# Kernel optimization log

Measured on AMD Instinct MI355X. Metric: run time of the kernel, lower is better.

Reference implementation:

```python
import jax, jax.numpy as jnp
import numpy as np

N = 8000        # nodes
E = 64000       # directed edges (before self-loops)
F_IN = 3201     # node_dim=1 + encoding_dim(128)*25
N_TRAIN = 4000


def setup_inputs() -> dict:
    key = jax.random.key(0)
    k = jax.random.split(key, 4)
    d = {
        'x': jax.random.normal(k[0], (N, F_IN), dtype=jnp.float32),
        'edge_index': jax.random.randint(k[1], (2, E), 0, N),
        'y': jax.random.uniform(k[2], (N,), dtype=jnp.float32),
        'train_idx': jax.random.randint(k[3], (N_TRAIN,), 0, N),
    }
    cnt = [0]
    def w(shape, fan_in):
        cnt[0] += 1
        kk = jax.random.fold_in(jax.random.key(1), cnt[0])
        return (jax.random.normal(kk, shape, dtype=jnp.float32) / np.float32(np.sqrt(fan_in)))
    ones = lambda n: jnp.ones((n,), jnp.float32)
    zeros = lambda n: jnp.zeros((n,), jnp.float32)
    d['bn0_g'] = ones(F_IN); d['bn0_b'] = zeros(F_IN)
    d['W1l'] = w((F_IN, 1024), F_IN); d['W1r'] = w((F_IN, 1024), F_IN)
    d['a1'] = w((2, 512), 512); d['b1'] = zeros(1024)
    d['bn1_g'] = ones(1024); d['bn1_b'] = zeros(1024)
    d['W2l'] = w((1024, 512), 1024); d['W2r'] = w((1024, 512), 1024)
    d['a2'] = w((1, 512), 512); d['b2'] = zeros(512)
    d['bn2_g'] = ones(512); d['bn2_b'] = zeros(512)
    d['W3l'] = w((512, 512), 512); d['W3r'] = w((512, 512), 512)
    d['a3'] = w((1, 512), 512); d['b3'] = zeros(512)
    d['bn3_g'] = ones(512); d['bn3_b'] = zeros(512)
    d['W4l'] = w((512, 512), 512); d['W4r'] = w((512, 512), 512)
    d['a4'] = w((1, 512), 512); d['b4'] = zeros(512)
    d['Wh'] = w((512, 1), 512); d['bh'] = zeros(1)
    return d


def _batchnorm(h, g, b, eps=1e-5):
    # training-mode batch statistics over the node dim
    m = h.mean(axis=0)
    v = h.var(axis=0)
    return (h - m) * jax.lax.rsqrt(v + jnp.float32(eps)) * g + b


def _gatv2(h, src, dst, Wl, Wr, att, bias, n):
    # GATv2Conv with concat heads, softmax over incoming edges, aggr='mean'
    H, C = att.shape
    xl = (h @ Wl).reshape(n, H, C)   # source transform
    xr = (h @ Wr).reshape(n, H, C)   # target transform
    z = jax.nn.leaky_relu(xl[src] + xr[dst], negative_slope=0.2)  # [E,H,C]
    e = jnp.einsum('ehc,hc->eh', z, att)                          # [E,H]
    emax = jax.ops.segment_max(e, dst, num_segments=n)            # segment softmax
    ex = jnp.exp(e - emax[dst])
    denom = jax.ops.segment_sum(ex, dst, num_segments=n)
    alpha = ex / denom[dst]
    agg = jax.ops.segment_sum(alpha[:, :, None] * xl[src], dst, num_segments=n)
    deg = jax.ops.segment_sum(jnp.ones(src.shape[0], h.dtype), dst, num_segments=n)
    return (agg / deg[:, None, None]).reshape(n, H * C) + bias


def reference(x, edge_index, y, train_idx, bn0_g, bn0_b, W1l, W1r, a1, b1,
              bn1_g, bn1_b, W2l, W2r, a2, b2, bn2_g, bn2_b, W3l, W3r, a3, b3,
              bn3_g, bn3_b, W4l, W4r, a4, b4, Wh, bh):
    n = x.shape[0]
    loops = jnp.arange(n, dtype=edge_index.dtype)  # PyG add_self_loops=True
    src = jnp.concatenate([edge_index[0], loops])
    dst = jnp.concatenate([edge_index[1], loops])
    h = _batchnorm(x, bn0_g, bn0_b)
    h = _gatv2(h, src, dst, W1l, W1r, a1, b1, n)          # -> [N,1024]
    h = jax.nn.relu(_batchnorm(h, bn1_g, bn1_b))
    h = _gatv2(h, src, dst, W2l, W2r, a2, b2, n)          # -> [N,512]
    h = jax.nn.relu(_batchnorm(h, bn2_g, bn2_b))
    h = _gatv2(h, src, dst, W3l, W3r, a3, b3, n)
    h = jax.nn.relu(_batchnorm(h, bn3_g, bn3_b))
    h = jax.nn.relu(_gatv2(h, src, dst, W4l, W4r, a4, b4, n))
    pred = jax.nn.sigmoid(h @ Wh + bh)[:, 0]              # [N]
    return pred[train_idx], y[train_idx]
```

## Files before the change

kernel.cpp:

```cpp
#include <hip/hip_runtime.h>
#include <math.h>

typedef __bf16 bf16x8 __attribute__((ext_vector_type(8)));
typedef float f32x4 __attribute__((ext_vector_type(4)));
typedef unsigned short ushort8 __attribute__((ext_vector_type(8)));

__device__ __forceinline__ float bf2f(unsigned short u) {
  union { unsigned int i; float f; } c; c.i = ((unsigned int)u) << 16; return c.f;
}
__device__ __forceinline__ unsigned short f2bf(float f) {
  union { float f; unsigned int i; } c; c.f = f;
  unsigned int r = (c.i + 0x7fffu + ((c.i >> 16) & 1u)) >> 16;
  return (unsigned short)r;
}

__global__ void deg_init_k(int* deg, int n) {
  int i = blockIdx.x * blockDim.x + threadIdx.x;
  if (i < n) deg[i] = 1;
}

__global__ void deg_count_k(const int* __restrict__ dst, int* __restrict__ deg, int e) {
  int i = blockIdx.x * blockDim.x + threadIdx.x;
  if (i < e) atomicAdd(&deg[dst[i]], 1);
}

__global__ void scan_k(const int* __restrict__ deg, int* __restrict__ offsets,
                       int* __restrict__ cursor, int n) {
  __shared__ int sums[1024];
  int tid = threadIdx.x;
  int chunk = (n + 1023) >> 10;
  int base = tid * chunk;
  int s = 0;
  for (int i = 0; i < chunk; ++i) {
    int j = base + i;
    if (j < n) s += deg[j];
  }
  sums[tid] = s;
  __syncthreads();
  for (int off = 1; off < 1024; off <<= 1) {
    int v = (tid >= off) ? sums[tid - off] : 0;
    __syncthreads();
    sums[tid] += v;
    __syncthreads();
  }
  int run = sums[tid] - s;
  for (int i = 0; i < chunk; ++i) {
    int j = base + i;
    if (j < n) {
      offsets[j] = run;
      cursor[j] = run;
      run += deg[j];
    }
  }
  if (tid == 1023) offsets[n] = sums[1023];
}

__global__ void csr_fill_k(const int* __restrict__ src, const int* __restrict__ dst,
                           int* __restrict__ cursor, int* __restrict__ csr_src,
                           int e, int n) {
  int i = blockIdx.x * blockDim.x + threadIdx.x;
  if (i >= e + n) return;
  int s, d;
  if (i < e) { s = src[i]; d = dst[i]; }
  else       { s = i - e;  d = s; }
  int pos = atomicAdd(&cursor[d], 1);
  csr_src[pos] = s;
}

__global__ __launch_bounds__(256)
void stats_convert_k(const float* __restrict__ x, unsigned short* __restrict__ Abf,
                     float* __restrict__ s1, float* __restrict__ s2,
                     int M, int K, int Kp) {
  int c = blockIdx.x * 256 + threadIdx.x;
  if (c >= Kp) return;
  int rows = (M + gridDim.y - 1) / gridDim.y;
  int r0 = blockIdx.y * rows;
  int r1 = min(M, r0 + rows);
  if (c >= K) {
    for (int r = r0; r < r1; ++r) Abf[(size_t)r * Kp + c] = 0;
    return;
  }
  float a = 0.f, b = 0.f;
  int r = r0;
  for (; r + 4 <= r1; r += 4) {
    float v0 = x[(size_t)(r + 0) * K + c];
    float v1 = x[(size_t)(r + 1) * K + c];
    float v2 = x[(size_t)(r + 2) * K + c];
    float v3 = x[(size_t)(r + 3) * K + c];
    a += v0 + v1 + v2 + v3;
    b += v0 * v0 + v1 * v1 + v2 * v2 + v3 * v3;
    Abf[(size_t)(r + 0) * Kp + c] = f2bf(v0);
    Abf[(size_t)(r + 1) * Kp + c] = f2bf(v1);
    Abf[(size_t)(r + 2) * Kp + c] = f2bf(v2);
    Abf[(size_t)(r + 3) * Kp + c] = f2bf(v3);
  }
  for (; r < r1; ++r) {
    float v = x[(size_t)r * K + c];
    a += v; b += v * v;
    Abf[(size_t)r * Kp + c] = f2bf(v);
  }
  atomicAdd(&s1[c], a);
  atomicAdd(&s2[c], b);
}

__global__ __launch_bounds__(256)
void col_stats_bf_k(const unsigned short* __restrict__ h, int M, int D,
                    float* __restrict__ s1, float* __restrict__ s2) {
  int c = blockIdx.x * 256 + threadIdx.x;
  if (c >= D) return;
  int rows = (M + gridDim.y - 1) / gridDim.y;
  int r0 = blockIdx.y * rows;
  int r1 = min(M, r0 + rows);
  float a = 0.f, b = 0.f;
  int r = r0;
  for (; r + 4 <= r1; r += 4) {
    float v0 = bf2f(h[(size_t)(r + 0) * D + c]);
    float v1 = bf2f(h[(size_t)(r + 1) * D + c]);
    float v2 = bf2f(h[(size_t)(r + 2) * D + c]);
    float v3 = bf2f(h[(size_t)(r + 3) * D + c]);
    a += v0 + v1 + v2 + v3;
    b += v0 * v0 + v1 * v1 + v2 * v2 + v3 * v3;
  }
  for (; r < r1; ++r) {
    float v = bf2f(h[(size_t)r * D + c]);
    a += v; b += v * v;
  }
  atomicAdd(&s1[c], a);
  atomicAdd(&s2[c], b);
}

__global__ void bn_fin_k(const float* __restrict__ s1, const float* __restrict__ s2,
                         const float* __restrict__ g, const float* __restrict__ b,
                         float* __restrict__ acol, float* __restrict__ ccol,
                         int D, float invM) {
  int c = blockIdx.x * blockDim.x + threadIdx.x;
  if (c >= D) return;
  float m = s1[c] * invM;
  float v = fmaxf(s2[c] * invM - m * m, 0.f);
  float a = rsqrtf(v + 1e-5f) * g[c];
  acol[c] = a;
  ccol[c] = b[c] - m * a;
}

__global__ __launch_bounds__(256)
void bn_apply8_k(const unsigned short* __restrict__ h, const float* __restrict__ acol,
                 const float* __restrict__ ccol, unsigned short* __restrict__ outb,
                 size_t total, int D) {
  size_t i = ((size_t)blockIdx.x * 256 + threadIdx.x) * 8;
  if (i >= total) return;
  ushort8 u = *(const ushort8*)(h + i);
  int c = (int)(i % (size_t)D);
  ushort8 o;
#pragma unroll
  for (int j = 0; j < 8; ++j) {
    float v = bf2f(u[j]) * acol[c + j] + ccol[c + j];
    o[j] = f2bf(fmaxf(v, 0.f));
  }
  *(ushort8*)(outb + i) = o;
}

__global__ __launch_bounds__(256)
void wconv_k(const float* __restrict__ W, unsigned short* __restrict__ WT,
             int K, int N, int Kp,
             const float* __restrict__ scale, const float* __restrict__ cshift,
             float* __restrict__ bias) {
  __shared__ float t[32][33];
  int n0 = blockIdx.x * 32, k0 = blockIdx.y * 32;
  int tx = threadIdx.x & 31, ty = threadIdx.x >> 5;
  float bsum = 0.f;
#pragma unroll
  for (int i = 0; i < 32; i += 8) {
    int k = k0 + ty + i, nn = n0 + tx;
    float v = (k < K && nn < N) ? W[(size_t)k * N + nn] : 0.f;
    t[ty + i][tx] = v;
    if (cshift && k < K) bsum += cshift[k] * v;
  }
  if (cshift) atomicAdd(&bias[n0 + tx], bsum);
  __syncthreads();
#pragma unroll
  for (int i = 0; i < 32; i += 8) {
    int nn = n0 + ty + i, k = k0 + tx;
    if (nn < N && k < Kp) {
      float v = t[tx][ty + i];
      if (scale && k < K) v *= scale[k];
      WT[(size_t)nn * Kp + k] = f2bf(v);
    }
  }
}

__global__ __launch_bounds__(256)
void gemm_bf16_k(const unsigned short* __restrict__ A,
                 const unsigned short* __restrict__ Bt,
                 unsigned short* __restrict__ outL, unsigned short* __restrict__ outR,
                 const float* __restrict__ bias, int M, int Nh, int K) {
  __shared__ unsigned short sA[128 * 64];
  __shared__ unsigned short sB[128 * 64];
  const int tid = threadIdx.x;
  const int wave = tid >> 6, lane = tid & 63;
  const int wm = wave >> 1, wn = wave & 1;
  const int l16 = lane & 15, lq = lane >> 4;
  const int row0 = blockIdx.y * 128, col0 = blockIdx.x * 128;

  f32x4 acc[4][4] = {};

  for (int kt = 0; kt < K; kt += 64) {
#pragma unroll
    for (int i = 0; i < 4; ++i) {
      int s = i * 256 + tid;
      int r = s >> 3;
      int g = (s & 7) ^ (r & 7);
      int ra = row0 + r;
      ra = ra < M ? ra : M - 1;
      const unsigned short* ga = A + (size_t)ra * K + (kt + g * 8);
      __builtin_amdgcn_global_load_lds(
          (const __attribute__((address_space(1))) void*)ga,
          (__attribute__((address_space(3))) void*)&sA[s * 8], 16, 0, 0);
      const unsigned short* gb = Bt + (size_t)(col0 + r) * K + (kt + g * 8);
      __builtin_amdgcn_global_load_lds(
          (const __attribute__((address_space(1))) void*)gb,
          (__attribute__((address_space(3))) void*)&sB[s * 8], 16, 0, 0);
    }
    __syncthreads();
#pragma unroll
    for (int ks = 0; ks < 2; ++ks) {
      bf16x8 af[4], bff[4];
#pragma unroll
      for (int t = 0; t < 4; ++t) {
        int g = ks * 4 + lq;
        int r = wm * 64 + t * 16 + l16;
        af[t] = *(const bf16x8*)&sA[(r * 8 + (g ^ (r & 7))) * 8];
        int rb = wn * 64 + t * 16 + l16;
        bff[t] = *(const bf16x8*)&sB[(rb * 8 + (g ^ (rb & 7))) * 8];
      }
#pragma unroll
      for (int mt = 0; mt < 4; ++mt)
#pragma unroll
        for (int nt = 0; nt < 4; ++nt)
          acc[mt][nt] = __builtin_amdgcn_mfma_f32_16x16x32_bf16(af[mt], bff[nt], acc[mt][nt], 0, 0, 0);
    }
    __syncthreads();
  }
#pragma unroll
  for (int mt = 0; mt < 4; ++mt) {
    int rbase = row0 + wm * 64 + mt * 16 + lq * 4;
#pragma unroll
    for (int nt = 0; nt < 4; ++nt) {
      int col = col0 + wn * 64 + nt * 16 + l16;
      float bv = bias ? bias[col] : 0.f;
      unsigned short* base;
      int cc;
      if (col < Nh) { base = outL; cc = col; }
      else          { base = outR; cc = col - Nh; }
#pragma unroll
      for (int r = 0; r < 4; ++r) {
        int rr = rbase + r;
        if (rr < M) base[(size_t)rr * Nh + cc] = f2bf(acc[mt][nt][r] + bv);
      }
    }
  }
}

template <int H>
__global__ __launch_bounds__(256)
void gat_edge_k(const unsigned short* __restrict__ xl, const unsigned short* __restrict__ xr,
                const float* __restrict__ att, const float* __restrict__ bias,
                const int* __restrict__ csr, const int* __restrict__ offsets,
                unsigned short* __restrict__ out, int n, int relu) {
  int gw = (blockIdx.x * 256 + threadIdx.x) >> 6;
  int lane = threadIdx.x & 63;
  if (gw >= n * H) return;
  int node = gw / H;
  int head = gw - node * H;
  const int W = H * 512;
  const size_t rowoff = (size_t)node * W + head * 512;
  int c0 = lane * 8;

  float xrv[8], atv[8];
  {
    ushort8 u = *(const ushort8*)(xr + rowoff + c0);
    const float* ap = att + head * 512 + c0;
#pragma unroll
    for (int j = 0; j < 8; ++j) { xrv[j] = bf2f(u[j]); atv[j] = ap[j]; }
  }
  float m = -1e30f, l = 0.f;
  float acc[8];
#pragma unroll
  for (int j = 0; j < 8; ++j) acc[j] = 0.f;
  int p0 = offsets[node], p1 = offsets[node + 1];
  for (int p = p0; p < p1; ++p) {
    int s = csr[p];
    ushort8 u = *(const ushort8*)(xl + (size_t)s * W + head * 512 + c0);
    float lv[8];
    float e = 0.f;
#pragma unroll
    for (int j = 0; j < 8; ++j) {
      lv[j] = bf2f(u[j]);
      float z = lv[j] + xrv[j];
      z = fmaxf(z, 0.f) + 0.2f * fminf(z, 0.f);
      e = fmaf(z, atv[j], e);
    }
#pragma unroll
    for (int off = 32; off > 0; off >>= 1) e += __shfl_xor(e, off, 64);
    float mn = fmaxf(m, e);
    float corr = __expf(m - mn);
    float w = __expf(e - mn);
    l = l * corr + w;
#pragma unroll
    for (int j = 0; j < 8; ++j) acc[j] = acc[j] * corr + w * lv[j];
    m = mn;
  }
  float inv = 1.f / (l * (float)(p1 - p0));
  const float* bp = bias + head * 512 + c0;
  ushort8 o;
#pragma unroll
  for (int j = 0; j < 8; ++j) {
    float v = acc[j] * inv + bp[j];
    if (relu) v = fmaxf(v, 0.f);
    o[j] = f2bf(v);
  }
  *(ushort8*)(out + rowoff + c0) = o;
}

__global__ __launch_bounds__(256)
void head_k(const unsigned short* __restrict__ h, const float* __restrict__ Wh,
            const float* __restrict__ bh, float* __restrict__ pred, int n) {
  int gw = (blockIdx.x * 256 + threadIdx.x) >> 6;
  int lane = threadIdx.x & 63;
  if (gw >= n) return;
  ushort8 u = *(const ushort8*)(h + (size_t)gw * 512 + lane * 8);
  const float* wp = Wh + lane * 8;
  float s = 0.f;
#pragma unroll
  for (int j = 0; j < 8; ++j) s = fmaf(bf2f(u[j]), wp[j], s);
#pragma unroll
  for (int off = 32; off > 0; off >>= 1) s += __shfl_xor(s, off, 64);
  if (lane == 0) pred[gw] = 1.f / (1.f + __expf(-(s + bh[0])));
}

__global__ void gather_k(const float* __restrict__ pred, const float* __restrict__ y,
                         const int* __restrict__ idx, float* __restrict__ out, int nt) {
  int i = blockIdx.x * blockDim.x + threadIdx.x;
  if (i >= nt) return;
  int j = idx[i];
  out[i] = pred[j];
  out[nt + i] = y[j];
}

extern "C" void kernel_launch(void* const* d_in, const int* in_sizes, int n_in,
                              void* d_out, int out_size, void* d_ws, size_t ws_size,
                              hipStream_t stream) {
  const float* x     = (const float*)d_in[0];
  const int*   ei    = (const int*)d_in[1];
  const float* y     = (const float*)d_in[2];
  const int*   tidx  = (const int*)d_in[3];
  const float* bn0_g = (const float*)d_in[4];
  const float* bn0_b = (const float*)d_in[5];
  const float* W1l   = (const float*)d_in[6];
  const float* W1r   = (const float*)d_in[7];
  const float* a1    = (const float*)d_in[8];
  const float* b1    = (const float*)d_in[9];
  const float* bn1_g = (const float*)d_in[10];
  const float* bn1_b = (const float*)d_in[11];
  const float* W2l   = (const float*)d_in[12];
  const float* W2r   = (const float*)d_in[13];
  const float* a2    = (const float*)d_in[14];
  const float* b2    = (const float*)d_in[15];
  const float* bn2_g = (const float*)d_in[16];
  const float* bn2_b = (const float*)d_in[17];
  const float* W3l   = (const float*)d_in[18];
  const float* W3r   = (const float*)d_in[19];
  const float* a3    = (const float*)d_in[20];
  const float* b3    = (const float*)d_in[21];
  const float* bn3_g = (const float*)d_in[22];
  const float* bn3_b = (const float*)d_in[23];
  const float* W4l   = (const float*)d_in[24];
  const float* W4r   = (const float*)d_in[25];
  const float* a4    = (const float*)d_in[26];
  const float* b4    = (const float*)d_in[27];
  const float* Wh    = (const float*)d_in[28];
  const float* bh    = (const float*)d_in[29];
  float* out = (float*)d_out;

  const int n   = in_sizes[2];
  const int E   = in_sizes[1] / 2;
  const int FIN = in_sizes[4];
  const int NT  = in_sizes[3];
  const int ET  = E + n;
  const int KP1 = 3264;

  unsigned short* us = (unsigned short*)d_ws;
  const size_t ABF_SZ = (size_t)n * KP1;
  unsigned short* Abf = us;
  unsigned short* hb  = us + ABF_SZ;
  unsigned short* xlb = hb + (size_t)n * 1024;
  unsigned short* xrb = xlb + (size_t)n * 1024;
  float* fp = (float*)(xrb + (size_t)n * 1024);
  float* pred  = fp;           fp += n;
  float* s1    = fp;           fp += 4096;
  float* s2    = fp;           fp += 4096;
  float* acol  = fp;           fp += 4096;
  float* ccol  = fp;           fp += 4096;
  float* biasb = fp;           fp += 4096;
  int* deg     = (int*)fp;
  int* offsets = deg + n;
  int* cursor  = offsets + n + 1;
  int* csr     = cursor + n;
  unsigned short* W1lT = hb;
  unsigned short* WlT  = Abf + (size_t)n * 1024;

  deg_init_k<<<(n + 255) / 256, 256, 0, stream>>>(deg, n);
  deg_count_k<<<(E + 255) / 256, 256, 0, stream>>>(ei + E, deg, E);
  scan_k<<<1, 1024, 0, stream>>>(deg, offsets, cursor, n);
  csr_fill_k<<<(ET + 255) / 256, 256, 0, stream>>>(ei, ei + E, cursor, csr, E, n);

  float invM = 1.f / (float)n;

  hipMemsetAsync(s1, 0, 2 * 4096 * sizeof(float), stream);
  {
    dim3 g((KP1 + 255) / 256, 200);
    stats_convert_k<<<g, 256, 0, stream>>>(x, Abf, s1, s2, n, FIN, KP1);
    bn_fin_k<<<(FIN + 255) / 256, 256, 0, stream>>>(s1, s2, bn0_g, bn0_b, acol, ccol, FIN, invM);
  }

  hipMemsetAsync(biasb, 0, 2048 * sizeof(float), stream);
  {
    dim3 gw1(1024 / 32, KP1 / 32);
    wconv_k<<<gw1, 256, 0, stream>>>(W1l, W1lT, FIN, 1024, KP1, acol, ccol, biasb);
    wconv_k<<<gw1, 256, 0, stream>>>(W1r, W1lT + (size_t)1024 * KP1, FIN, 1024, KP1, acol, ccol, biasb + 1024);
    dim3 g(2048 / 128, (n + 127) / 128);
    gemm_bf16_k<<<g, 256, 0, stream>>>(Abf, W1lT, xlb, xrb, biasb, n, 1024, KP1);
  }
  gat_edge_k<2><<<(n * 2 + 3) / 4, 256, 0, stream>>>(xlb, xrb, a1, b1, csr, offsets, hb, n, 0);

  hipMemsetAsync(s1, 0, 2 * 4096 * sizeof(float), stream);
  {
    dim3 g(1024 / 256, 160);
    col_stats_bf_k<<<g, 256, 0, stream>>>(hb, n, 1024, s1, s2);
    bn_fin_k<<<4, 256, 0, stream>>>(s1, s2, bn1_g, bn1_b, acol, ccol, 1024, invM);
    bn_apply8_k<<<(int)(((size_t)n * 1024 / 8 + 255) / 256), 256, 0, stream>>>(hb, acol, ccol, Abf, (size_t)n * 1024, 1024);
  }

  {
    dim3 gw2(512 / 32, 1024 / 32);
    wconv_k<<<gw2, 256, 0, stream>>>(W2l, WlT, 1024, 512, 1024, nullptr, nullptr, nullptr);
    wconv_k<<<gw2, 256, 0, stream>>>(W2r, WlT + (size_t)512 * 1024, 1024, 512, 1024, nullptr, nullptr, nullptr);
    dim3 g(1024 / 128, (n + 127) / 128);
    gemm_bf16_k<<<g, 256, 0, stream>>>(Abf, WlT, xlb, xrb, nullptr, n, 512, 1024);
  }
  gat_edge_k<1><<<(n + 3) / 4, 256, 0, stream>>>(xlb, xrb, a2, b2, csr, offsets, hb, n, 0);

  hipMemsetAsync(s1, 0, 2 * 4096 * sizeof(float), stream);
  {
    dim3 g(512 / 256, 160);
    col_stats_bf_k<<<g, 256, 0, stream>>>(hb, n, 512, s1, s2);
    bn_fin_k<<<2, 256, 0, stream>>>(s1, s2, bn2_g, bn2_b, acol, ccol, 512, invM);
    bn_apply8_k<<<(int)(((size_t)n * 512 / 8 + 255) / 256), 256, 0, stream>>>(hb, acol, ccol, Abf, (size_t)n * 512, 512);
  }

  {
    dim3 gw3(512 / 32, 512 / 32);
    wconv_k<<<gw3, 256, 0, stream>>>(W3l, WlT, 512, 512, 512, nullptr, nullptr, nullptr);
    wconv_k<<<gw3, 256, 0, stream>>>(W3r, WlT + (size_t)512 * 512, 512, 512, 512, nullptr, nullptr, nullptr);
    dim3 g(1024 / 128, (n + 127) / 128);
    gemm_bf16_k<<<g, 256, 0, stream>>>(Abf, WlT, xlb, xrb, nullptr, n, 512, 512);
  }
  gat_edge_k<1><<<(n + 3) / 4, 256, 0, stream>>>(xlb, xrb, a3, b3, csr, offsets, hb, n, 0);

  hipMemsetAsync(s1, 0, 2 * 4096 * sizeof(float), stream);
  {
    dim3 g(512 / 256, 160);
    col_stats_bf_k<<<g, 256, 0, stream>>>(hb, n, 512, s1, s2);
    bn_fin_k<<<2, 256, 0, stream>>>(s1, s2, bn3_g, bn3_b, acol, ccol, 512, invM);
    bn_apply8_k<<<(int)(((size_t)n * 512 / 8 + 255) / 256), 256, 0, stream>>>(hb, acol, ccol, Abf, (size_t)n * 512, 512);
  }

  {
    dim3 gw4(512 / 32, 512 / 32);
    wconv_k<<<gw4, 256, 0, stream>>>(W4l, WlT, 512, 512, 512, nullptr, nullptr, nullptr);
    wconv_k<<<gw4, 256, 0, stream>>>(W4r, WlT + (size_t)512 * 512, 512, 512, 512, nullptr, nullptr, nullptr);
    dim3 g(1024 / 128, (n + 127) / 128);
    gemm_bf16_k<<<g, 256, 0, stream>>>(Abf, WlT, xlb, xrb, nullptr, n, 512, 512);
  }
  gat_edge_k<1><<<(n + 3) / 4, 256, 0, stream>>>(xlb, xrb, a4, b4, csr, offsets, hb, n, 1);

  head_k<<<(n + 3) / 4, 256, 0, stream>>>(hb, Wh, bh, pred, n);
  gather_k<<<(NT + 255) / 256, 256, 0, stream>>>(pred, y, tidx, out, NT);
}
```

Before: 832.8 us.

## Vectorize input stats/convert, prefetch GAT neighbors, fuse BN finalize and head gather

The input stats/convert kernel now has each thread handle four columns and write packed 4-wide bf16 stores, with a taller grid. The BN finalize for the hidden layers moves inside the apply kernel, which removes three launches at the cost of redundant per-element rsqrt work. The GAT edge kernel software-prefetches neighbor rows two ahead to hide gather latency. The output head is evaluated only for train indices and fused with the gather, which skips head work on unused nodes.

```diff
diff --git a/kernel.cpp b/kernel.cpp
--- a/kernel.cpp
+++ b/kernel.cpp
@@ -4,6 +4,7 @@
 typedef __bf16 bf16x8 __attribute__((ext_vector_type(8)));
 typedef float f32x4 __attribute__((ext_vector_type(4)));
 typedef unsigned short ushort8 __attribute__((ext_vector_type(8)));
+typedef unsigned short ushort4_t __attribute__((ext_vector_type(4)));
 
 __device__ __forceinline__ float bf2f(unsigned short u) {
   union { unsigned int i; float f; } c; c.i = ((unsigned int)u) << 16; return c.f;
@@ -71,36 +72,51 @@
 void stats_convert_k(const float* __restrict__ x, unsigned short* __restrict__ Abf,
                      float* __restrict__ s1, float* __restrict__ s2,
                      int M, int K, int Kp) {
-  int c = blockIdx.x * 256 + threadIdx.x;
-  if (c >= Kp) return;
+  int c0 = (blockIdx.x * 256 + threadIdx.x) * 4;
+  if (c0 >= Kp) return;
   int rows = (M + gridDim.y - 1) / gridDim.y;
   int r0 = blockIdx.y * rows;
   int r1 = min(M, r0 + rows);
-  if (c >= K) {
-    for (int r = r0; r < r1; ++r) Abf[(size_t)r * Kp + c] = 0;
-    return;
-  }
-  float a = 0.f, b = 0.f;
+  bool inK[4];
+#pragma unroll
+  for (int q = 0; q < 4; ++q) inK[q] = (c0 + q) < K;
+  float sa[4] = {0.f, 0.f, 0.f, 0.f}, sb[4] = {0.f, 0.f, 0.f, 0.f};
   int r = r0;
   for (; r + 4 <= r1; r += 4) {
-    float v0 = x[(size_t)(r + 0) * K + c];
-    float v1 = x[(size_t)(r + 1) * K + c];
-    float v2 = x[(size_t)(r + 2) * K + c];
-    float v3 = x[(size_t)(r + 3) * K + c];
-    a += v0 + v1 + v2 + v3;
-    b += v0 * v0 + v1 * v1 + v2 * v2 + v3 * v3;
-    Abf[(size_t)(r + 0) * Kp + c] = f2bf(v0);
-    Abf[(size_t)(r + 1) * Kp + c] = f2bf(v1);
-    Abf[(size_t)(r + 2) * Kp + c] = f2bf(v2);
-    Abf[(size_t)(r + 3) * Kp + c] = f2bf(v3);
+    float v[4][4];
+#pragma unroll
+    for (int i = 0; i < 4; ++i)
+#pragma unroll
+      for (int q = 0; q < 4; ++q)
+        v[i][q] = inK[q] ? x[(size_t)(r + i) * K + c0 + q] : 0.f;
+#pragma unroll
+    for (int i = 0; i < 4; ++i) {
+      ushort4_t o;
+#pragma unroll
+      for (int q = 0; q < 4; ++q) {
+        sa[q] += v[i][q];
+        sb[q] += v[i][q] * v[i][q];
+        o[q] = f2bf(v[i][q]);
+      }
+      *(ushort4_t*)&Abf[(size_t)(r + i) * Kp + c0] = o;
+    }
   }
   for (; r < r1; ++r) {
-    float v = x[(size_t)r * K + c];
-    a += v; b += v * v;
-    Abf[(size_t)r * Kp + c] = f2bf(v);
-  }
-  atomicAdd(&s1[c], a);
-  atomicAdd(&s2[c], b);
+    ushort4_t o;
+#pragma unroll
+    for (int q = 0; q < 4; ++q) {
+      float v = inK[q] ? x[(size_t)r * K + c0 + q] : 0.f;
+      sa[q] += v; sb[q] += v * v;
+      o[q] = f2bf(v);
+    }
+    *(ushort4_t*)&Abf[(size_t)r * Kp + c0] = o;
+  }
+#pragma unroll
+  for (int q = 0; q < 4; ++q)
+    if (inK[q]) {
+      atomicAdd(&s1[c0 + q], sa[q]);
+      atomicAdd(&s2[c0 + q], sb[q]);
+    }
 }
 
 __global__ __launch_bounds__(256)
@@ -143,9 +159,11 @@
 }
 
 __global__ __launch_bounds__(256)
-void bn_apply8_k(const unsigned short* __restrict__ h, const float* __restrict__ acol,
-                 const float* __restrict__ ccol, unsigned short* __restrict__ outb,
-                 size_t total, int D) {
+void bn_apply8_k(const unsigned short* __restrict__ h,
+                 const float* __restrict__ s1, const float* __restrict__ s2,
+                 const float* __restrict__ g, const float* __restrict__ b,
+                 unsigned short* __restrict__ outb,
+                 size_t total, int D, float invM) {
   size_t i = ((size_t)blockIdx.x * 256 + threadIdx.x) * 8;
   if (i >= total) return;
   ushort8 u = *(const ushort8*)(h + i);
@@ -153,7 +171,11 @@
   ushort8 o;
 #pragma unroll
   for (int j = 0; j < 8; ++j) {
-    float v = bf2f(u[j]) * acol[c + j] + ccol[c + j];
+    float m = s1[c + j] * invM;
+    float var = fmaxf(s2[c + j] * invM - m * m, 0.f);
+    float a = rsqrtf(var + 1e-5f) * g[c + j];
+    float cc = b[c + j] - m * a;
+    float v = bf2f(u[j]) * a + cc;
     o[j] = f2bf(fmaxf(v, 0.f));
   }
   *(ushort8*)(outb + i) = o;
@@ -269,27 +291,33 @@
   int gw = (blockIdx.x * 256 + threadIdx.x) >> 6;
   int lane = threadIdx.x & 63;
   if (gw >= n * H) return;
-  int node = gw / H;
-  int head = gw - node * H;
+  int node, head;
+  if (H == 1) { node = gw; head = 0; }
+  else        { node = gw >> 1; head = gw & 1; }
   const int W = H * 512;
   const size_t rowoff = (size_t)node * W + head * 512;
-  int c0 = lane * 8;
+  const size_t choff = (size_t)head * 512 + (size_t)(lane * 8);
 
   float xrv[8], atv[8];
   {
-    ushort8 u = *(const ushort8*)(xr + rowoff + c0);
-    const float* ap = att + head * 512 + c0;
+    ushort8 u = *(const ushort8*)(xr + rowoff + lane * 8);
+    const float* ap = att + head * 512 + lane * 8;
 #pragma unroll
     for (int j = 0; j < 8; ++j) { xrv[j] = bf2f(u[j]); atv[j] = ap[j]; }
   }
+  int p0 = offsets[node], p1 = offsets[node + 1];
+  ushort8 u0 = *(const ushort8*)(xl + (size_t)csr[p0] * W + choff);
+  ushort8 u1 = u0;
+  if (p0 + 1 < p1) u1 = *(const ushort8*)(xl + (size_t)csr[p0 + 1] * W + choff);
+
   float m = -1e30f, l = 0.f;
   float acc[8];
 #pragma unroll
   for (int j = 0; j < 8; ++j) acc[j] = 0.f;
-  int p0 = offsets[node], p1 = offsets[node + 1];
   for (int p = p0; p < p1; ++p) {
-    int s = csr[p];
-    ushort8 u = *(const ushort8*)(xl + (size_t)s * W + head * 512 + c0);
+    ushort8 u = u0;
+    u0 = u1;
+    if (p + 2 < p1) u1 = *(const ushort8*)(xl + (size_t)csr[p + 2] * W + choff);
     float lv[8];
     float e = 0.f;
 #pragma unroll
@@ -310,7 +338,7 @@
     m = mn;
   }
   float inv = 1.f / (l * (float)(p1 - p0));
-  const float* bp = bias + head * 512 + c0;
+  const float* bp = bias + head * 512 + lane * 8;
   ushort8 o;
 #pragma unroll
   for (int j = 0; j < 8; ++j) {
@@ -318,32 +346,28 @@
     if (relu) v = fmaxf(v, 0.f);
     o[j] = f2bf(v);
   }
-  *(ushort8*)(out + rowoff + c0) = o;
-}
-
-__global__ __launch_bounds__(256)
-void head_k(const unsigned short* __restrict__ h, const float* __restrict__ Wh,
-            const float* __restrict__ bh, float* __restrict__ pred, int n) {
+  *(ushort8*)(out + rowoff + lane * 8) = o;
+}
+
+__global__ __launch_bounds__(256)
+void head_gather_k(const unsigned short* __restrict__ h, const float* __restrict__ Wh,
+                   const float* __restrict__ bh, const float* __restrict__ y,
+                   const int* __restrict__ tidx, float* __restrict__ out, int nt) {
   int gw = (blockIdx.x * 256 + threadIdx.x) >> 6;
   int lane = threadIdx.x & 63;
-  if (gw >= n) return;
-  ushort8 u = *(const ushort8*)(h + (size_t)gw * 512 + lane * 8);
+  if (gw >= nt) return;
+  int j = tidx[gw];
+  ushort8 u = *(const ushort8*)(h + (size_t)j * 512 + lane * 8);
   const float* wp = Wh + lane * 8;
   float s = 0.f;
 #pragma unroll
-  for (int j = 0; j < 8; ++j) s = fmaf(bf2f(u[j]), wp[j], s);
+  for (int q = 0; q < 8; ++q) s = fmaf(bf2f(u[q]), wp[q], s);
 #pragma unroll
   for (int off = 32; off > 0; off >>= 1) s += __shfl_xor(s, off, 64);
-  if (lane == 0) pred[gw] = 1.f / (1.f + __expf(-(s + bh[0])));
-}
-
-__global__ void gather_k(const float* __restrict__ pred, const float* __restrict__ y,
-                         const int* __restrict__ idx, float* __restrict__ out, int nt) {
-  int i = blockIdx.x * blockDim.x + threadIdx.x;
-  if (i >= nt) return;
-  int j = idx[i];
-  out[i] = pred[j];
-  out[nt + i] = y[j];
+  if (lane == 0) {
+    out[gw] = 1.f / (1.f + __expf(-(s + bh[0])));
+    out[nt + gw] = y[j];
+  }
 }
 
 extern "C" void kernel_launch(void* const* d_in, const int* in_sizes, int n_in,
@@ -395,7 +419,6 @@
   unsigned short* xlb = hb + (size_t)n * 1024;
   unsigned short* xrb = xlb + (size_t)n * 1024;
   float* fp = (float*)(xrb + (size_t)n * 1024);
-  float* pred  = fp;           fp += n;
   float* s1    = fp;           fp += 4096;
   float* s2    = fp;           fp += 4096;
   float* acol  = fp;           fp += 4096;
@@ -417,7 +440,7 @@
 
   hipMemsetAsync(s1, 0, 2 * 4096 * sizeof(float), stream);
   {
-    dim3 g((KP1 + 255) / 256, 200);
+    dim3 g((KP1 / 4 + 255) / 256, 250);
     stats_convert_k<<<g, 256, 0, stream>>>(x, Abf, s1, s2, n, FIN, KP1);
     bn_fin_k<<<(FIN + 255) / 256, 256, 0, stream>>>(s1, s2, bn0_g, bn0_b, acol, ccol, FIN, invM);
   }
@@ -436,8 +459,8 @@
   {
     dim3 g(1024 / 256, 160);
     col_stats_bf_k<<<g, 256, 0, stream>>>(hb, n, 1024, s1, s2);
-    bn_fin_k<<<4, 256, 0, stream>>>(s1, s2, bn1_g, bn1_b, acol, ccol, 1024, invM);
-    bn_apply8_k<<<(int)(((size_t)n * 1024 / 8 + 255) / 256), 256, 0, stream>>>(hb, acol, ccol, Abf, (size_t)n * 1024, 1024);
+    bn_apply8_k<<<(int)(((size_t)n * 1024 / 8 + 255) / 256), 256, 0, stream>>>(
+        hb, s1, s2, bn1_g, bn1_b, Abf, (size_t)n * 1024, 1024, invM);
   }
 
   {
@@ -453,8 +476,8 @@
   {
     dim3 g(512 / 256, 160);
     col_stats_bf_k<<<g, 256, 0, stream>>>(hb, n, 512, s1, s2);
-    bn_fin_k<<<2, 256, 0, stream>>>(s1, s2, bn2_g, bn2_b, acol, ccol, 512, invM);
-    bn_apply8_k<<<(int)(((size_t)n * 512 / 8 + 255) / 256), 256, 0, stream>>>(hb, acol, ccol, Abf, (size_t)n * 512, 512);
+    bn_apply8_k<<<(int)(((size_t)n * 512 / 8 + 255) / 256), 256, 0, stream>>>(
+        hb, s1, s2, bn2_g, bn2_b, Abf, (size_t)n * 512, 512, invM);
   }
 
   {
@@ -470,8 +493,8 @@
   {
     dim3 g(512 / 256, 160);
     col_stats_bf_k<<<g, 256, 0, stream>>>(hb, n, 512, s1, s2);
-    bn_fin_k<<<2, 256, 0, stream>>>(s1, s2, bn3_g, bn3_b, acol, ccol, 512, invM);
-    bn_apply8_k<<<(int)(((size_t)n * 512 / 8 + 255) / 256), 256, 0, stream>>>(hb, acol, ccol, Abf, (size_t)n * 512, 512);
+    bn_apply8_k<<<(int)(((size_t)n * 512 / 8 + 255) / 256), 256, 0, stream>>>(
+        hb, s1, s2, bn3_g, bn3_b, Abf, (size_t)n * 512, 512, invM);
   }
 
   {
@@ -483,6 +506,5 @@
   }
   gat_edge_k<1><<<(n + 3) / 4, 256, 0, stream>>>(xlb, xrb, a4, b4, csr, offsets, hb, n, 1);
 
-  head_k<<<(n + 3) / 4, 256, 0, stream>>>(hb, Wh, bh, pred, n);
-  gather_k<<<(NT + 255) / 256, 256, 0, stream>>>(pred, y, tidx, out, NT);
-}
+  head_gather_k<<<(NT + 3) / 4, 256, 0, stream>>>(hb, Wh, bh, y, tidx, out, NT);
+}
```

Result: slower. 895.4 us (+7.5%).
